# Optimization experiments

Measured on AMD Instinct MI355X. Metric: run time of the kernel, lower is better.

Reference implementation:

```python
import jax, jax.numpy as jnp
from jax import lax
import numpy as np

RATIO = 2
KF = 12  # FIR kernel size = 6 * ratio


def _kaiser_sinc_filter(cutoff, half_width, ksize):
    # matches BigVGAN alias_free_torch kaiser_sinc_filter1d (even ksize branch)
    half_size = ksize // 2
    delta_f = 4.0 * half_width
    A = 2.285 * (half_size - 1) * np.pi * delta_f + 7.95
    if A > 50.0:
        beta = 0.1102 * (A - 8.7)
    elif A >= 21.0:
        beta = 0.5842 * (A - 21.0) ** 0.4 + 0.07886 * (A - 21.0)
    else:
        beta = 0.0
    window = np.kaiser(ksize, beta)
    time = np.arange(-half_size, half_size) + 0.5
    filt = 2 * cutoff * window * np.sinc(2 * cutoff * time)
    filt = filt / filt.sum()
    return filt.astype(np.float32)


FILT = jnp.asarray(_kaiser_sinc_filter(0.5 / RATIO, 0.6 / RATIO, KF))  # [12], symmetric


def _depthwise(x, stride, lhs_dil, pad):
    # x: [B, C, T]; same FIR filter applied per channel
    C = x.shape[1]
    w = jnp.broadcast_to(FILT.reshape(1, 1, KF), (C, 1, KF))
    return lax.conv_general_dilated(
        x, w, window_strides=(stride,), padding=[pad], lhs_dilation=(lhs_dil,),
        dimension_numbers=('NCH', 'OIH', 'NCH'), feature_group_count=C)


def _activation1d(x, log_alpha, log_beta):
    # anti-aliased SnakeBeta: upsample x2 -> snake -> downsample x2 (length preserved)
    # UpSample1d(ratio=2): replicate-pad 5, conv_transpose stride 2, crop 15 each side
    x = jnp.pad(x, ((0, 0), (0, 0), (5, 5)), mode='edge')
    x = RATIO * _depthwise(x, stride=1, lhs_dil=RATIO, pad=(KF - 1, KF - 1))
    x = x[..., 15:-15]  # [B, C, 2T]
    a = jnp.exp(log_alpha)[None, :, None]
    b = jnp.exp(log_beta)[None, :, None]
    x = x + (1.0 / (b + 1e-9)) * jnp.square(jnp.sin(x * a))
    # DownSample1d: replicate-pad (5, 6), conv stride 2
    x = jnp.pad(x, ((0, 0), (0, 0), (5, 6)), mode='edge')
    return _depthwise(x, stride=RATIO, lhs_dil=1, pad=(0, 0))


def _wn_conv(x, v, g, b, d):
    # weight_norm: w = g * v / ||v||_(in,k) per output channel; dilated, 'same' padding
    w = g * v * lax.rsqrt(jnp.sum(v * v, axis=(1, 2), keepdims=True))
    y = lax.conv_general_dilated(
        x, w, window_strides=(1,), padding=[(d, d)], rhs_dilation=(d,),
        dimension_numbers=('NCH', 'OIH', 'NCH'))
    return y + b[None, :, None]


def setup_inputs() -> dict:
    key = jax.random.key(0)
    ks = jax.random.split(key, 4)
    B, C, T, L = 8, 512, 8192, 3
    x = jax.random.normal(ks[0], (B, C, T), jnp.float32)
    conv_v = 0.01 * jax.random.normal(ks[1], (L, C, C, 3), jnp.float32)  # init_weights std=0.01
    conv_g = jnp.ones((L, C, 1, 1), jnp.float32)
    conv_b = jnp.zeros((L, C), jnp.float32)
    alpha = 0.1 * jax.random.normal(ks[2], (L, C), jnp.float32)  # log-scale snake params
    beta = 0.1 * jax.random.normal(ks[3], (L, C), jnp.float32)
    return {'x': x, 'conv_v': conv_v, 'conv_g': conv_g, 'conv_b': conv_b,
            'alpha': alpha, 'beta': beta}


def reference(x, conv_v, conv_g, conv_b, alpha, beta):
    for i, d in enumerate((1, 3, 5)):
        xt = _activation1d(x, alpha[i], beta[i])
        xt = _wn_conv(xt, conv_v[i], conv_g[i], conv_b[i], d)
        x = xt + x
    return x
```

## Files before the change

kernel.cpp:

```cpp
#include <hip/hip_runtime.h>
#include <hip/hip_bf16.h>
#include <cmath>

#define CCH 512
#define TLEN 8192
#define NB 8
#define KFILT 12

typedef unsigned short u16;
typedef __attribute__((ext_vector_type(8))) short short8;
typedef __attribute__((ext_vector_type(8))) unsigned short ushort8;
typedef __attribute__((ext_vector_type(4))) float float4v;
typedef __attribute__((ext_vector_type(4))) int int4v;

struct Filt { float f[KFILT]; };

static double bessel_i0(double x) {
    double sum = 1.0, term = 1.0;
    for (int k = 1; k < 40; ++k) {
        double t = (x * 0.5) / k;
        term *= t * t;
        sum += term;
        if (term < 1e-18 * sum) break;
    }
    return sum;
}

static void make_filter(float* out) {
    const int ksize = KFILT, half = KFILT / 2;
    const double cutoff = 0.5 / 2.0;
    const double half_width = 0.6 / 2.0;
    const double delta_f = 4.0 * half_width;
    const double PI = 3.14159265358979323846;
    double A = 2.285 * (half - 1) * PI * delta_f + 7.95;
    double beta;
    if (A > 50.0) beta = 0.1102 * (A - 8.7);
    else if (A >= 21.0) beta = 0.5842 * pow(A - 21.0, 0.4) + 0.07886 * (A - 21.0);
    else beta = 0.0;
    double i0b = bessel_i0(beta);
    double sum = 0.0, f[KFILT];
    for (int n = 0; n < ksize; ++n) {
        double r = (2.0 * n) / (ksize - 1) - 1.0;
        double w = bessel_i0(beta * sqrt(fmax(0.0, 1.0 - r * r))) / i0b;
        double t = (n - half) + 0.5;
        double xx = 2.0 * cutoff * t;
        double snc = (xx == 0.0) ? 1.0 : sin(PI * xx) / (PI * xx);
        f[n] = 2.0 * cutoff * w * snc;
        sum += f[n];
    }
    for (int n = 0; n < ksize; ++n) out[n] = (float)(f[n] / sum);
}

__device__ __forceinline__ float bf2f(u16 u) {
    return __uint_as_float(((unsigned int)u) << 16);
}
__device__ __forceinline__ u16 f2bf(float f) {
    unsigned int x = __float_as_uint(f);
    unsigned int r = (x + 0x7fffu + ((x >> 16) & 1u)) >> 16;
    return (u16)r;
}
__device__ __forceinline__ float ldin(const void* p, size_t i, int isf) {
    return isf ? ((const float*)p)[i] : bf2f(((const u16*)p)[i]);
}
__device__ __forceinline__ void gl_lds16(const void* g, void* s) {
    __builtin_amdgcn_global_load_lds(
        (const __attribute__((address_space(1))) unsigned int*)g,
        (__attribute__((address_space(3))) unsigned int*)s, 16, 0, 0);
}

__global__ __launch_bounds__(256) void k_detect(const u16* __restrict__ x,
                                                int* __restrict__ flag) {
    int tid = threadIdx.x;
    int bad = 0;
    for (int i = tid; i < 4096; i += 256) {
        int e = (x[i] >> 7) & 0xFF;
        if (e >= 0x86) bad++;
    }
    for (int off = 32; off > 0; off >>= 1) bad += __shfl_down(bad, off, 64);
    __shared__ int r[4];
    if ((tid & 63) == 0) r[tid >> 6] = bad;
    __syncthreads();
    if (tid == 0) flag[0] = (r[0] + r[1] + r[2] + r[3] >= 64) ? 1 : 0;
}

__global__ __launch_bounds__(256) void k_scales(const void* __restrict__ v,
                                                const void* __restrict__ g,
                                                float* __restrict__ scales,
                                                const int* __restrict__ flg) {
    int isf = *flg;
    int blk = blockIdx.x;
    int tid = threadIdx.x;
    float s = 0.f;
    for (int i = tid; i < CCH * 3; i += 256) {
        float x = ldin(v, (size_t)blk * (CCH * 3) + i, isf);
        s = fmaf(x, x, s);
    }
    for (int off = 32; off > 0; off >>= 1) s += __shfl_down(s, off, 64);
    __shared__ float red[4];
    if ((tid & 63) == 0) red[tid >> 6] = s;
    __syncthreads();
    if (tid == 0) {
        float tot = red[0] + red[1] + red[2] + red[3];
        scales[blk] = ldin(g, blk, isf) / sqrtf(tot);
    }
}

__global__ __launch_bounds__(256) void k_repack(const void* __restrict__ v,
                                                u16* __restrict__ wp,
                                                const int* __restrict__ flg) {
    int isf = *flg;
    int l = blockIdx.y;
    int i = blockIdx.x * 256 + threadIdx.x;
    int tap = i >> 18;
    int rem = i & 262143;
    int co = rem >> 9, ci = rem & 511;
    size_t src = (((size_t)l * CCH + co) * CCH + ci) * 3 + tap;
    u16 val = isf ? f2bf(((const float*)v)[src]) : ((const u16*)v)[src];
    wp[(((size_t)l * 3 + tap) * CCH + co) * CCH + ci] = val;
}

template<int UL>
__device__ __forceinline__ float su_val(const float* xr, const Filt& F,
                                        float a, float invb) {
    constexpr int S = (UL < 0) ? -(((-UL) + 1) / 2) : (UL / 2);
    constexpr int P = ((UL % 2) + 2) % 2;
    constexpr int B = S + (P ? 4 : 3);
    float acc = F.f[P] * xr[B];
    #pragma unroll
    for (int r = 1; r < 6; ++r) acc = fmaf(F.f[2 * r + P], xr[B + r], acc);
    acc *= 2.0f;
    float sn = __sinf(acc * a);
    return fmaf(invb, sn * sn, acc);
}

__global__ __launch_bounds__(256) void k_act(const void* __restrict__ xsrc,
                                             const void* __restrict__ alpha,
                                             const void* __restrict__ beta,
                                             int prmofs, u16* __restrict__ xt,
                                             Filt F, const int* __restrict__ flg,
                                             int layer0) {
    const int isf = *flg;
    const int sif = layer0 ? isf : 0;
    const int tid = threadIdx.x;
    const int lane = tid & 63, w = tid >> 6;
    const int b = blockIdx.z;
    const int c = blockIdx.y * 64 + lane;
    const int t0 = blockIdx.x * 128 + w * 32;
    const size_t rowbase = ((size_t)(b * CCH + c)) * TLEN;

    const float a = expf(ldin(alpha, prmofs + c, isf));
    const float invb = 1.0f / (expf(ldin(beta, prmofs + c, isf)) + 1e-9f);

    float xr[44];
    const bool interior = (t0 != 0) && (t0 != TLEN - 32);
    if (sif) {
        const float* xp = (const float*)xsrc + rowbase;
        if (interior) {
            #pragma unroll
            for (int i = 0; i < 12; ++i) {
                float4v v = *(const float4v*)(xp + t0 - 8 + i * 4);
                #pragma unroll
                for (int j = 0; j < 4; ++j) {
                    int k = i * 4 + j - 2;
                    if (k >= 0 && k < 44) xr[k] = v[j];
                }
            }
        } else {
            #pragma unroll
            for (int k = 0; k < 44; ++k)
                xr[k] = xp[min(max(t0 - 6 + k, 0), TLEN - 1)];
        }
    } else {
        const u16* xp = (const u16*)xsrc + rowbase;
        if (interior) {
            #pragma unroll
            for (int i = 0; i < 6; ++i) {
                ushort8 v = *(const ushort8*)(xp + t0 - 8 + i * 8);
                #pragma unroll
                for (int j = 0; j < 8; ++j) {
                    int k = i * 8 + j - 2;
                    if (k >= 0 && k < 44) xr[k] = bf2f(v[j]);
                }
            }
        } else {
            #pragma unroll
            for (int k = 0; k < 44; ++k)
                xr[k] = bf2f(xp[min(max(t0 - 6 + k, 0), TLEN - 1)]);
        }
    }

    float wv[12];
    wv[7]  = su_val<-5>(xr, F, a, invb);
    wv[8]  = su_val<-4>(xr, F, a, invb);
    wv[9]  = su_val<-3>(xr, F, a, invb);
    wv[10] = su_val<-2>(xr, F, a, invb);
    wv[11] = su_val<-1>(xr, F, a, invb);
    wv[0]  = su_val<0>(xr, F, a, invb);
    wv[1]  = su_val<1>(xr, F, a, invb);
    wv[2]  = su_val<2>(xr, F, a, invb);
    wv[3]  = su_val<3>(xr, F, a, invb);
    wv[4]  = su_val<4>(xr, F, a, invb);
    wv[5]  = su_val<5>(xr, F, a, invb);
    wv[6]  = su_val<6>(xr, F, a, invb);
    if (t0 == 0) { wv[7] = wv[8] = wv[9] = wv[10] = wv[11] = wv[0]; }
    const bool right = (t0 == TLEN - 32);
    const float su_hi = su_val<63>(xr, F, a, invb);

    u16* orow = xt + (size_t)b * TLEN * CCH + c;

#define IDXW(u) ((((u) % 12) + 12) % 12)
#define ACT_STEP(TL) { \
      float acc = F.f[0] * wv[IDXW(2*(TL)-5)]; \
      acc = fmaf(F.f[1],  wv[IDXW(2*(TL)-4)], acc); \
      acc = fmaf(F.f[2],  wv[IDXW(2*(TL)-3)], acc); \
      acc = fmaf(F.f[3],  wv[IDXW(2*(TL)-2)], acc); \
      acc = fmaf(F.f[4],  wv[IDXW(2*(TL)-1)], acc); \
      acc = fmaf(F.f[5],  wv[IDXW(2*(TL)+0)], acc); \
      acc = fmaf(F.f[6],  wv[IDXW(2*(TL)+1)], acc); \
      acc = fmaf(F.f[7],  wv[IDXW(2*(TL)+2)], acc); \
      acc = fmaf(F.f[8],  wv[IDXW(2*(TL)+3)], acc); \
      acc = fmaf(F.f[9],  wv[IDXW(2*(TL)+4)], acc); \
      acc = fmaf(F.f[10], wv[IDXW(2*(TL)+5)], acc); \
      acc = fmaf(F.f[11], wv[IDXW(2*(TL)+6)], acc); \
      orow[(size_t)(t0 + (TL)) * CCH] = f2bf(acc); \
      if ((TL) < 31) { \
        float nv1 = su_val<2*(TL)+7>(xr, F, a, invb); \
        float nv2 = su_val<2*(TL)+8>(xr, F, a, invb); \
        if ((2*(TL)+7) > 63) nv1 = right ? su_hi : nv1; \
        if ((2*(TL)+8) > 63) nv2 = right ? su_hi : nv2; \
        wv[IDXW(2*(TL)+7)] = nv1; \
        wv[IDXW(2*(TL)+8)] = nv2; \
      } \
    }

    ACT_STEP(0)  ACT_STEP(1)  ACT_STEP(2)  ACT_STEP(3)
    ACT_STEP(4)  ACT_STEP(5)  ACT_STEP(6)  ACT_STEP(7)
    ACT_STEP(8)  ACT_STEP(9)  ACT_STEP(10) ACT_STEP(11)
    ACT_STEP(12) ACT_STEP(13) ACT_STEP(14) ACT_STEP(15)
    ACT_STEP(16) ACT_STEP(17) ACT_STEP(18) ACT_STEP(19)
    ACT_STEP(20) ACT_STEP(21) ACT_STEP(22) ACT_STEP(23)
    ACT_STEP(24) ACT_STEP(25) ACT_STEP(26) ACT_STEP(27)
    ACT_STEP(28) ACT_STEP(29) ACT_STEP(30) ACT_STEP(31)
#undef ACT_STEP
#undef IDXW
}

__global__ __launch_bounds__(256) void k_conv(const u16* __restrict__ xt,
                                              const u16* __restrict__ wp,
                                              const float* __restrict__ scales,
                                              const void* __restrict__ bias,
                                              int bofs,
                                              const void* __restrict__ rsrc,
                                              int layer0,
                                              u16* __restrict__ wdst,
                                              void* __restrict__ outp, int d,
                                              const int* __restrict__ flg) {
    extern __shared__ char smem[];
    const int isf = *flg;
    const int rif = layer0 ? isf : 0;
    const int tid = threadIdx.x;
    const int lane = tid & 63, wid = tid >> 6;
    const int wm = wid & 1, wn = wid >> 1;
    const int b = blockIdx.z, co0 = blockIdx.y * 128, t0 = blockIdx.x * 128;
    const int q = lane >> 4, l15 = lane & 15;
    const int nX = (128 + 2 * d) * 4;
    const bool edge = (t0 == 0) || (t0 + 128 == TLEN);
    const u16* xtb = xt + (size_t)b * TLEN * CCH;

    float4v acc[4][4];
    #pragma unroll
    for (int i = 0; i < 4; ++i)
        #pragma unroll
        for (int j = 0; j < 4; ++j) acc[i][j] = (float4v){0.f, 0.f, 0.f, 0.f};

    auto stageA = [&](int ci0, char* As) {
        #pragma unroll
        for (int i = 0; i < 6; ++i) {
            int base = (i * 4 + wid) * 64;
            int L = base + lane;
            int tap = L >> 9;
            int co = (L >> 2) & 127;
            int g = (L & 3) ^ ((co >> 1) & 3);
            gl_lds16(wp + (((size_t)tap * CCH + co0 + co) * CCH + ci0 + g * 8),
                     As + base * 16);
        }
    };
    auto stageX = [&](int ci0, char* Xs) {
        #pragma unroll
        for (int i = 0; i < 3; ++i) {
            int base = (i * 4 + wid) * 64;
            int L = base + lane;
            int t = L >> 2;
            int g = (L & 3) ^ ((t >> 1) & 3);
            int tg = min(max(t0 - d + t, 0), TLEN - 1);
            gl_lds16(xtb + ((size_t)tg * CCH + ci0 + g * 8), Xs + base * 16);
        }
    };
    auto fixX = [&](char* Xs) {
        for (int j = tid; j < nX; j += 256) {
            int tg = t0 - d + (j >> 2);
            if (tg < 0 || tg >= TLEN)
                *(int4v*)(Xs + (size_t)j * 16) = (int4v){0, 0, 0, 0};
        }
    };

    stageA(0, smem);
    stageX(0, smem + 49152);
    __syncthreads();
    if (edge) { fixX(smem + 49152); __syncthreads(); }

    #pragma unroll 2
    for (int s = 0; s < 16; ++s) {
        const int cur = s & 1, nxt = cur ^ 1;
        char* As = smem + cur * 24576;
        char* Xs = smem + 49152 + cur * 12288;
        if (s < 15) {
            stageA((s + 1) * 32, smem + nxt * 24576);
            stageX((s + 1) * 32, smem + 49152 + nxt * 12288);
        }
        #pragma unroll
        for (int tap = 0; tap < 3; ++tap) {
            short8 af[4], bfr[4];
            #pragma unroll
            for (int mi = 0; mi < 4; ++mi) {
                int co = wm * 64 + mi * 16 + l15;
                af[mi] = *(const short8*)(As + tap * 8192 + co * 64 +
                                          ((q ^ ((co >> 1) & 3)) * 16));
            }
            #pragma unroll
            for (int ni = 0; ni < 4; ++ni) {
                int r = wn * 64 + ni * 16 + l15 + tap * d;
                bfr[ni] = *(const short8*)(Xs + r * 64 + ((q ^ ((r >> 1) & 3)) * 16));
            }
            #pragma unroll
            for (int mi = 0; mi < 4; ++mi)
                #pragma unroll
                for (int ni = 0; ni < 4; ++ni)
                    acc[mi][ni] = __builtin_amdgcn_mfma_f32_16x16x32_bf16(
                        af[mi], bfr[ni], acc[mi][ni], 0, 0, 0);
        }
        __syncthreads();
        if (edge && s < 15) {
            fixX(smem + 49152 + nxt * 12288);
            __syncthreads();
        }
    }

    float scl[4][4], bia[4][4];
    #pragma unroll
    for (int mi = 0; mi < 4; ++mi)
        #pragma unroll
        for (int rg = 0; rg < 4; ++rg) {
            int co = co0 + wm * 64 + mi * 16 + q * 4 + rg;
            scl[mi][rg] = scales[co];
            bia[mi][rg] = ldin(bias, bofs + co, isf);
        }
    #pragma unroll
    for (int mi = 0; mi < 4; ++mi)
        #pragma unroll
        for (int ni = 0; ni < 4; ++ni) {
            int tg = t0 + wn * 64 + ni * 16 + l15;
            #pragma unroll
            for (int rg = 0; rg < 4; ++rg) {
                int co = co0 + wm * 64 + mi * 16 + q * 4 + rg;
                size_t idx = ((size_t)(b * CCH + co)) * TLEN + tg;
                float resid = rif ? ((const float*)rsrc)[idx]
                                  : bf2f(((const u16*)rsrc)[idx]);
                float val = fmaf(acc[mi][ni][rg], scl[mi][rg], bia[mi][rg]) + resid;
                if (wdst) {
                    wdst[idx] = f2bf(val);
                } else {
                    if (isf) ((float*)outp)[idx] = val;
                    else ((u16*)outp)[idx] = f2bf(val);
                }
            }
        }
}

extern "C" void kernel_launch(void* const* d_in, const int* in_sizes, int n_in,
                              void* d_out, int out_size, void* d_ws, size_t ws_size,
                              hipStream_t stream) {
    const void* x_in  = d_in[0];
    const void* v_in  = d_in[1];
    const void* g_in  = d_in[2];
    const void* b_in  = d_in[3];
    const void* al_in = d_in[4];
    const void* be_in = d_in[5];

    char* ws = (char*)d_ws;
    u16*   xc     = (u16*)ws;
    u16*   xt     = (u16*)(ws + 67108864);
    u16*   wp     = (u16*)(ws + 134217728);
    float* scales = (float*)(ws + 134217728 + 4718592);
    int*   flag   = (int*)(ws + 134217728 + 4718592 + 6144);

    Filt F;
    make_filter(F.f);

    (void)hipFuncSetAttribute((const void*)k_conv,
                              hipFuncAttributeMaxDynamicSharedMemorySize, 73728);

    k_detect<<<1, 256, 0, stream>>>((const u16*)x_in, flag);
    k_scales<<<3 * CCH, 256, 0, stream>>>(v_in, g_in, scales, flag);
    k_repack<<<dim3(3072, 3), 256, 0, stream>>>(v_in, wp, flag);

    const int dil[3] = {1, 3, 5};
    for (int l = 0; l < 3; ++l) {
        const void* src = (l == 0) ? x_in : (const void*)xc;
        k_act<<<dim3(TLEN / 128, CCH / 64, NB), 256, 0, stream>>>(
            src, al_in, be_in, l * CCH, xt, F, flag, (l == 0) ? 1 : 0);
        k_conv<<<dim3(TLEN / 128, CCH / 128, NB), 256, 73728, stream>>>(
            xt, wp + (size_t)l * 3 * CCH * CCH, scales + l * CCH, b_in, l * CCH,
            src, (l == 0) ? 1 : 0,
            (l == 2) ? (u16*)nullptr : xc,
            (l == 2) ? d_out : nullptr, dil[l], flag);
    }
}
```

Baseline: 831.8 us.

## Load conv weight fragments directly from global memory instead of staging in LDS

The conv kernel no longer stages the weight (A) tiles through shared memory. Each lane reads its MFMA weight fragments straight from global memory (cached in L2), so LDS drops to 24 KB of double-buffered X tiles. A launch-bounds occupancy hint of 4 blocks is also added. The aim is to cut LDS traffic and footprint so more blocks fit per CU. The cost is many more global and cache loads on the MFMA critical path, with no prefetch for the weight fragments.

```diff
diff --git a/kernel.cpp b/kernel.cpp
--- a/kernel.cpp
+++ b/kernel.cpp
@@ -245,7 +245,7 @@
 #undef IDXW
 }
 
-__global__ __launch_bounds__(256) void k_conv(const u16* __restrict__ xt,
+__global__ __launch_bounds__(256, 4) void k_conv(const u16* __restrict__ xt,
                                               const u16* __restrict__ wp,
                                               const float* __restrict__ scales,
                                               const void* __restrict__ bias,
@@ -255,7 +255,7 @@
                                               u16* __restrict__ wdst,
                                               void* __restrict__ outp, int d,
                                               const int* __restrict__ flg) {
-    extern __shared__ char smem[];
+    __shared__ __align__(16) char Xsm[2][12288];
     const int isf = *flg;
     const int rif = layer0 ? isf : 0;
     const int tid = threadIdx.x;
@@ -267,34 +267,28 @@
     const bool edge = (t0 == 0) || (t0 + 128 == TLEN);
     const u16* xtb = xt + (size_t)b * TLEN * CCH;
 
+    const u16* wbase = wp + ((size_t)(co0 + wm * 64 + l15)) * CCH + q * 8;
+
+    const u16* xsrc3[3];
+    #pragma unroll
+    for (int i = 0; i < 3; ++i) {
+        int L = (i * 4 + wid) * 64 + lane;
+        int t = L >> 2;
+        int g = (L & 3) ^ ((t >> 1) & 3);
+        int tg = min(max(t0 - d + t, 0), TLEN - 1);
+        xsrc3[i] = xtb + (size_t)tg * CCH + g * 8;
+    }
+
     float4v acc[4][4];
     #pragma unroll
     for (int i = 0; i < 4; ++i)
         #pragma unroll
         for (int j = 0; j < 4; ++j) acc[i][j] = (float4v){0.f, 0.f, 0.f, 0.f};
 
-    auto stageA = [&](int ci0, char* As) {
-        #pragma unroll
-        for (int i = 0; i < 6; ++i) {
-            int base = (i * 4 + wid) * 64;
-            int L = base + lane;
-            int tap = L >> 9;
-            int co = (L >> 2) & 127;
-            int g = (L & 3) ^ ((co >> 1) & 3);
-            gl_lds16(wp + (((size_t)tap * CCH + co0 + co) * CCH + ci0 + g * 8),
-                     As + base * 16);
-        }
-    };
     auto stageX = [&](int ci0, char* Xs) {
         #pragma unroll
-        for (int i = 0; i < 3; ++i) {
-            int base = (i * 4 + wid) * 64;
-            int L = base + lane;
-            int t = L >> 2;
-            int g = (L & 3) ^ ((t >> 1) & 3);
-            int tg = min(max(t0 - d + t, 0), TLEN - 1);
-            gl_lds16(xtb + ((size_t)tg * CCH + ci0 + g * 8), Xs + base * 16);
-        }
+        for (int i = 0; i < 3; ++i)
+            gl_lds16(xsrc3[i] + ci0, Xs + (i * 4 + wid) * 64 * 16);
     };
     auto fixX = [&](char* Xs) {
         for (int j = tid; j < nX; j += 256) {
@@ -304,29 +298,22 @@
         }
     };
 
-    stageA(0, smem);
-    stageX(0, smem + 49152);
+    stageX(0, Xsm[0]);
     __syncthreads();
-    if (edge) { fixX(smem + 49152); __syncthreads(); }
+    if (edge) { fixX(Xsm[0]); __syncthreads(); }
 
     #pragma unroll 2
     for (int s = 0; s < 16; ++s) {
-        const int cur = s & 1, nxt = cur ^ 1;
-        char* As = smem + cur * 24576;
-        char* Xs = smem + 49152 + cur * 12288;
-        if (s < 15) {
-            stageA((s + 1) * 32, smem + nxt * 24576);
-            stageX((s + 1) * 32, smem + 49152 + nxt * 12288);
-        }
+        const int cur = s & 1;
+        const char* Xs = Xsm[cur];
+        if (s < 15) stageX((s + 1) * 32, Xsm[cur ^ 1]);
         #pragma unroll
         for (int tap = 0; tap < 3; ++tap) {
             short8 af[4], bfr[4];
             #pragma unroll
-            for (int mi = 0; mi < 4; ++mi) {
-                int co = wm * 64 + mi * 16 + l15;
-                af[mi] = *(const short8*)(As + tap * 8192 + co * 64 +
-                                          ((q ^ ((co >> 1) & 3)) * 16));
-            }
+            for (int mi = 0; mi < 4; ++mi)
+                af[mi] = *(const short8*)(wbase + (size_t)tap * 262144 +
+                                          mi * 8192 + s * 32);
             #pragma unroll
             for (int ni = 0; ni < 4; ++ni) {
                 int r = wn * 64 + ni * 16 + l15 + tap * d;
@@ -341,7 +328,7 @@
         }
         __syncthreads();
         if (edge && s < 15) {
-            fixX(smem + 49152 + nxt * 12288);
+            fixX(Xsm[cur ^ 1]);
             __syncthreads();
         }
     }
@@ -397,9 +384,6 @@
     Filt F;
     make_filter(F.f);
 
-    (void)hipFuncSetAttribute((const void*)k_conv,
-                              hipFuncAttributeMaxDynamicSharedMemorySize, 73728);
-
     k_detect<<<1, 256, 0, stream>>>((const u16*)x_in, flag);
     k_scales<<<3 * CCH, 256, 0, stream>>>(v_in, g_in, scales, flag);
     k_repack<<<dim3(3072, 3), 256, 0, stream>>>(v_in, wp, flag);
@@ -409,7 +393,7 @@
         const void* src = (l == 0) ? x_in : (const void*)xc;
         k_act<<<dim3(TLEN / 128, CCH / 64, NB), 256, 0, stream>>>(
             src, al_in, be_in, l * CCH, xt, F, flag, (l == 0) ? 1 : 0);
-        k_conv<<<dim3(TLEN / 128, CCH / 128, NB), 256, 73728, stream>>>(
+        k_conv<<<dim3(TLEN / 128, CCH / 128, NB), 256, 0, stream>>>(
             xt, wp + (size_t)l * 3 * CCH * CCH, scales + l * CCH, b_in, l * CCH,
             src, (l == 0) ? 1 : 0,
             (l == 2) ? (u16*)nullptr : xc,
```

Result: slower. 1.202 ms (+44.4%).
